# Kernel optimization log

Measured on AMD Instinct MI355X. Metric: run time of the kernel, lower is better.

The kernel has to match this reference:

```python
import jax, jax.numpy as jnp
import numpy as np

B, C, L = 8, 512, 2048
HEADS, DIM_HEAD = 8, 64
HID = HEADS * DIM_HEAD  # 512


def setup_inputs() -> dict:
    key = jax.random.key(0)
    k1, k2, k3, k4 = jax.random.split(key, 4)
    x = jax.random.normal(k1, (B, C, L), dtype=jnp.float32)
    # Conv1d kernel_size=1 weights stored as [out, in] matrices
    w_qkv = jax.random.normal(k2, (3 * HID, C), dtype=jnp.float32) * (1.0 / np.sqrt(C))
    w_out = jax.random.normal(k3, (C, HID), dtype=jnp.float32) * (1.0 / np.sqrt(HID))
    b_out = jax.random.normal(k4, (C,), dtype=jnp.float32) * 0.01
    return {"x": x, "w_qkv": w_qkv, "w_out": w_out, "b_out": b_out}


def reference(x, w_qkv, w_out, b_out):
    scale = DIM_HEAD ** (-0.5)
    # 1x1 conv == channel-wise linear: [b,c,l] -> [b,3*hid,l]
    qkv = jnp.einsum('oc,bcl->bol', w_qkv, x)
    q, k, v = jnp.split(qkv, 3, axis=1)
    # split heads: b (h d) l -> b h d l
    split = lambda t: t.reshape(x.shape[0], HEADS, DIM_HEAD, t.shape[-1])
    q, k, v = split(q) * scale, split(k), split(v)
    sim = jnp.einsum('bhdi,bhdj->bhij', q, k)  # [b,h,l,l]
    attn = jax.nn.softmax(sim, axis=-1)
    out = jnp.einsum('bhij,bhdj->bhid', attn, v)  # [b,h,l,d]
    # b h l d -> b (h d) l
    out = jnp.transpose(out, (0, 1, 3, 2)).reshape(x.shape[0], HID, x.shape[-1])
    return jnp.einsum('oc,bcl->bol', w_out, out) + b_out[None, :, None]
```

## Files before the change

### kernel.cpp

```cpp
#include <hip/hip_runtime.h>

#define NB 8
#define NC 512
#define NL 2048
#define NH 8
#define ND 64
#define NHID 512

typedef float f32x4 __attribute__((ext_vector_type(4)));
typedef short bf16x8 __attribute__((ext_vector_type(8)));
typedef unsigned uint32x2 __attribute__((ext_vector_type(2)));
typedef unsigned uint32x4 __attribute__((ext_vector_type(4)));

__device__ __forceinline__ unsigned short f2bf(float x) {
    unsigned u = __float_as_uint(x);
    u += 0x7fffu + ((u >> 16) & 1u);
    return (unsigned short)(u >> 16);
}

__device__ __forceinline__ unsigned pack_bf16_tr(float lo, float hi) {
#if __has_builtin(__builtin_amdgcn_perm)
    return __builtin_amdgcn_perm(__float_as_uint(hi), __float_as_uint(lo), 0x07060302u);
#else
    return (__float_as_uint(lo) >> 16) | (__float_as_uint(hi) & 0xffff0000u);
#endif
}

__device__ __forceinline__ float fexp2(float x) {
#if __has_builtin(__builtin_amdgcn_exp2f)
    return __builtin_amdgcn_exp2f(x);
#else
    return exp2f(x);
#endif
}

__device__ __forceinline__ void gll16(const unsigned short* g, unsigned short* l) {
    __builtin_amdgcn_global_load_lds(
        (const __attribute__((address_space(1))) unsigned int*)g,
        (__attribute__((address_space(3))) unsigned int*)l, 16, 0, 0);
}

__device__ __forceinline__ void pfr_quad_swap(unsigned &a, unsigned &b) {
#if __has_builtin(__builtin_amdgcn_permlane32_swap) && __has_builtin(__builtin_amdgcn_permlane16_swap)
    uint32x2 r0 = __builtin_amdgcn_permlane32_swap(a, b, false, false);
    uint32x2 r1 = __builtin_amdgcn_permlane16_swap(r0[0], r0[1], false, false);
    a = r1[0];
    b = r1[1];
#else
    const int lane = (int)(threadIdx.x & 63);
    const int li = lane & 15, quad = lane >> 4;
    const int s0 = (li + ((quad & 1) << 5)) << 2;
    const int s1 = (li + 16 + ((quad & 1) << 5)) << 2;
    int ra = __builtin_amdgcn_ds_bpermute(s0, (int)a);
    int rb = __builtin_amdgcn_ds_bpermute(s0, (int)b);
    int ta = __builtin_amdgcn_ds_bpermute(s1, (int)a);
    int tb = __builtin_amdgcn_ds_bpermute(s1, (int)b);
    const bool lo = quad < 2;
    a = (unsigned)(lo ? ra : rb);
    b = (unsigned)(lo ? ta : tb);
#endif
}

__global__ __launch_bounds__(256) void xpose_kernel(
    const float* __restrict__ x, unsigned short* __restrict__ xT)
{
    __shared__ unsigned short T[64 * 65];
    const int tid = threadIdx.x;
    const int l0 = blockIdx.x * 64, c0 = blockIdx.y * 64, b = blockIdx.z;

    const int ll = tid & 63, cl0 = tid >> 6;
    #pragma unroll
    for (int i = 0; i < 16; i++) {
        const int cl = cl0 + 4 * i;
        T[cl * 65 + ll] = f2bf(x[((size_t)(b * NC + c0 + cl)) * NL + l0 + ll]);
    }
    __syncthreads();
    const int cg = tid & 7, lr = tid >> 3;
    #pragma unroll
    for (int rep = 0; rep < 2; rep++) {
        const int l = lr + rep * 32;
        unsigned u[4];
        #pragma unroll
        for (int j = 0; j < 4; j++) {
            unsigned short a = T[(cg * 8 + 2 * j) * 65 + l];
            unsigned short c = T[(cg * 8 + 2 * j + 1) * 65 + l];
            u[j] = (unsigned)a | ((unsigned)c << 16);
        }
        uint4 val; val.x = u[0]; val.y = u[1]; val.z = u[2]; val.w = u[3];
        *(uint4*)&xT[((size_t)(b * NL + l0 + l)) * NC + c0 + cg * 8] = val;
    }
}

__global__ __launch_bounds__(256) void wconv_kernel(
    const float* __restrict__ src, unsigned short* __restrict__ dst,
    int n8, int nscale8, float scale)
{
    const int idx = blockIdx.x * 256 + threadIdx.x;
    if (idx >= n8) return;
    const float s = (idx < nscale8) ? scale : 1.0f;
    float4 a = *(const float4*)&src[(size_t)idx * 8];
    float4 c = *(const float4*)&src[(size_t)idx * 8 + 4];
    uint4 val;
    val.x = (unsigned)f2bf(a.x * s) | ((unsigned)f2bf(a.y * s) << 16);
    val.y = (unsigned)f2bf(a.z * s) | ((unsigned)f2bf(a.w * s) << 16);
    val.z = (unsigned)f2bf(c.x * s) | ((unsigned)f2bf(c.y * s) << 16);
    val.w = (unsigned)f2bf(c.z * s) | ((unsigned)f2bf(c.w * s) << 16);
    *(uint4*)&dst[(size_t)idx * 8] = val;
}

__global__ __launch_bounds__(256) void qkv_proj_kernel(
    const unsigned short* __restrict__ xT, const unsigned short* __restrict__ wq,
    unsigned short* __restrict__ qb, unsigned short* __restrict__ kb,
    unsigned short* __restrict__ vb)
{
    __shared__ __align__(16) unsigned short Xt[128 * 64];
    __shared__ __align__(16) unsigned short Wt[128 * 64];
    const int tid = threadIdx.x;
    const int wave = tid >> 6, lane = tid & 63;
    const int quad = lane >> 4, li = lane & 15;
    const int o0 = blockIdx.x * 128, l0 = blockIdx.y * 128, b = blockIdx.z;

    const f32x4 fzero = {0.f, 0.f, 0.f, 0.f};
    f32x4 acc[2][8];
    #pragma unroll
    for (int mt = 0; mt < 2; mt++)
        #pragma unroll
        for (int nt = 0; nt < 8; nt++) acc[mt][nt] = fzero;

    const int srow = lane >> 3, schk = lane & 7;

    for (int c0 = 0; c0 < NC; c0 += 64) {
        #pragma unroll
        for (int i = 0; i < 4; i++) {
            const int r = wave * 32 + i * 8 + srow;
            gll16(xT + ((size_t)(b * NL + l0 + r)) * NC + c0 + ((schk ^ (r & 7)) * 8),
                  &Xt[(wave * 32 + i * 8) * 64]);
            gll16(wq + (size_t)(o0 + r) * NC + c0 + ((schk ^ (r & 7)) * 8),
                  &Wt[(wave * 32 + i * 8) * 64]);
        }
        __syncthreads();
        #pragma unroll
        for (int kc = 0; kc < 2; kc++) {
            const int sw = ((kc * 4 + quad) ^ (li & 7)) * 8;
            bf16x8 afr0 = *(const bf16x8*)&Xt[(wave * 32 + li) * 64 + sw];
            bf16x8 afr1 = *(const bf16x8*)&Xt[(wave * 32 + 16 + li) * 64 + sw];
            #pragma unroll
            for (int nt = 0; nt < 8; nt++) {
                bf16x8 bfr = *(const bf16x8*)&Wt[(nt * 16 + li) * 64 + sw];
                acc[0][nt] = __builtin_amdgcn_mfma_f32_16x16x32_bf16(afr0, bfr, acc[0][nt], 0, 0, 0);
                acc[1][nt] = __builtin_amdgcn_mfma_f32_16x16x32_bf16(afr1, bfr, acc[1][nt], 0, 0, 0);
            }
        }
        __syncthreads();
    }

    const int lr0 = l0 + wave * 32;
    if (o0 < 1024) {
        unsigned short* dst = (o0 < 512) ? qb : kb;
        #pragma unroll
        for (int mt = 0; mt < 2; mt++)
            #pragma unroll
            for (int nt = 0; nt < 8; nt++) {
                int oc = (o0 & 511) + nt * 16 + li;
                int hh = oc >> 6, d = oc & 63;
                size_t base =
                    ((size_t)((b * NH + hh) * NL) + lr0 + mt * 16 + quad * 4) * ND + d;
                #pragma unroll
                for (int r = 0; r < 4; r++)
                    dst[base + (size_t)r * ND] = f2bf(acc[mt][nt][r]);
            }
    } else {
        #pragma unroll
        for (int mt = 0; mt < 2; mt++)
            #pragma unroll
            for (int nt = 0; nt < 8; nt++) {
                int oc = (o0 - 1024) + nt * 16 + li;
                int hh = oc >> 6, d = oc & 63;
                size_t base = ((size_t)((b * NH + hh) * ND) + d) * NL +
                              lr0 + mt * 16 + quad * 4;
                uint2 pv;
                pv.x = (unsigned)f2bf(acc[mt][nt][0]) | ((unsigned)f2bf(acc[mt][nt][1]) << 16);
                pv.y = (unsigned)f2bf(acc[mt][nt][2]) | ((unsigned)f2bf(acc[mt][nt][3]) << 16);
                *(uint2*)&vb[base] = pv;
            }
    }
}

__global__ __launch_bounds__(256, 4) void attn_kernel(
    const unsigned short* __restrict__ qb, const unsigned short* __restrict__ kb,
    const unsigned short* __restrict__ vb, unsigned short* __restrict__ at)
{
    __shared__ __align__(16) unsigned short Kt[2][64 * 64];
    __shared__ __align__(16) unsigned short Vt[2][64 * 64];
    const int tid = threadIdx.x;
    const int wave = tid >> 6, lane = tid & 63;
    const int quad = lane >> 4, li = lane & 15;

    const int dlin = (int)(blockIdx.x + 16 * (blockIdx.y + 8 * blockIdx.z));
    const int xcd = dlin & 7, slot = dlin >> 3;
    const int qt = slot & 15, gidx = slot >> 4;
    const int g = xcd + 8 * gidx;
    const int h = g & 7, b = g >> 3;

    const int bh = b * NH + h;
    const unsigned short* Qb = qb + (size_t)bh * NL * ND;
    const unsigned short* Kb = kb + (size_t)bh * NL * ND;
    const unsigned short* Vb = vb + (size_t)bh * ND * NL;

    bf16x8 qfr[2][2];
    #pragma unroll
    for (int mt = 0; mt < 2; mt++)
        #pragma unroll
        for (int kc = 0; kc < 2; kc++)
            qfr[mt][kc] = *(const bf16x8*)&Qb[(size_t)(qt * 128 + wave * 32 + mt * 16 + li) * ND +
                                             kc * 32 + quad * 8];

    const f32x4 fzero = {0.f, 0.f, 0.f, 0.f};
    f32x4 oacc[2][4];
    #pragma unroll
    for (int mt = 0; mt < 2; mt++)
        #pragma unroll
        for (int dt = 0; dt < 4; dt++) oacc[mt][dt] = fzero;

    f32x4 lsacc0 = fzero, lsacc1 = fzero;
    const short one_bf = (short)0x3F80;
    const bf16x8 ones = {one_bf, one_bf, one_bf, one_bf,
                         one_bf, one_bf, one_bf, one_bf};

    const int rrow = lane >> 3;
    const int rchk = lane & 7;

    auto stage = [&](int buf, int j0) {
        #pragma unroll
        for (int i = 0; i < 2; i++) {
            const int jrow = wave * 16 + i * 8 + rrow;
            gll16(Kb + (size_t)(j0 + jrow) * ND + ((rchk ^ (jrow & 7)) * 8),
                  &Kt[buf][(wave * 16 + i * 8) * 64]);
            const int drow = wave * 16 + i * 8 + rrow;
            gll16(Vb + (size_t)drow * NL + j0 + ((rchk ^ (drow & 7)) * 8),
                  &Vt[buf][(wave * 16 + i * 8) * 64]);
        }
    };

    stage(0, 0);
    __syncthreads();

    #pragma unroll 2
    for (int kt = 0; kt < 32; kt++) {
        const int cur = kt & 1;
        if (kt < 31) stage(cur ^ 1, (kt + 1) * 64);

        __builtin_amdgcn_s_setprio(1);
        #pragma unroll
        for (int c = 0; c < 2; c++) {
            f32x4 st00 = fzero, st01 = fzero, st10 = fzero, st11 = fzero;
            #pragma unroll
            for (int dk = 0; dk < 2; dk++) {
                const int sw = ((dk * 4 + quad) ^ (li & 7)) * 8;
                bf16x8 kf0 = *(const bf16x8*)&Kt[cur][((2 * c + 0) * 16 + li) * 64 + sw];
                bf16x8 kf1 = *(const bf16x8*)&Kt[cur][((2 * c + 1) * 16 + li) * 64 + sw];
                st00 = __builtin_amdgcn_mfma_f32_16x16x32_bf16(kf0, qfr[0][dk], st00, 0, 0, 0);
                st01 = __builtin_amdgcn_mfma_f32_16x16x32_bf16(kf1, qfr[0][dk], st01, 0, 0, 0);
                st10 = __builtin_amdgcn_mfma_f32_16x16x32_bf16(kf0, qfr[1][dk], st10, 0, 0, 0);
                st11 = __builtin_amdgcn_mfma_f32_16x16x32_bf16(kf1, qfr[1][dk], st11, 0, 0, 0);
            }

            unsigned p000, p001, p010, p011, p100, p101, p110, p111;
            {
                float a0 = fexp2(st00[0]), a1 = fexp2(st00[1]),
                      a2 = fexp2(st00[2]), a3 = fexp2(st00[3]);
                float b0 = fexp2(st01[0]), b1 = fexp2(st01[1]),
                      b2 = fexp2(st01[2]), b3 = fexp2(st01[3]);
                p000 = pack_bf16_tr(a0, a1); p001 = pack_bf16_tr(a2, a3);
                p010 = pack_bf16_tr(b0, b1); p011 = pack_bf16_tr(b2, b3);
            }
            {
                float a0 = fexp2(st10[0]), a1 = fexp2(st10[1]),
                      a2 = fexp2(st10[2]), a3 = fexp2(st10[3]);
                float b0 = fexp2(st11[0]), b1 = fexp2(st11[1]),
                      b2 = fexp2(st11[2]), b3 = fexp2(st11[3]);
                p100 = pack_bf16_tr(a0, a1); p101 = pack_bf16_tr(a2, a3);
                p110 = pack_bf16_tr(b0, b1); p111 = pack_bf16_tr(b2, b3);
            }

            pfr_quad_swap(p000, p010);
            pfr_quad_swap(p001, p011);
            pfr_quad_swap(p100, p110);
            pfr_quad_swap(p101, p111);

            uint32x4 u0 = {p000, p001, p010, p011};
            uint32x4 u1 = {p100, p101, p110, p111};
            bf16x8 pf0 = __builtin_bit_cast(bf16x8, u0);
            bf16x8 pf1 = __builtin_bit_cast(bf16x8, u1);

            lsacc0 = __builtin_amdgcn_mfma_f32_16x16x32_bf16(ones, pf0, lsacc0, 0, 0, 0);
            lsacc1 = __builtin_amdgcn_mfma_f32_16x16x32_bf16(ones, pf1, lsacc1, 0, 0, 0);

            #pragma unroll
            for (int dt = 0; dt < 4; dt++) {
                const int swv = ((c * 4 + quad) ^ (li & 7)) * 8;
                bf16x8 vfr = *(const bf16x8*)&Vt[cur][(dt * 16 + li) * 64 + swv];
                oacc[0][dt] = __builtin_amdgcn_mfma_f32_16x16x32_bf16(vfr, pf0, oacc[0][dt], 0, 0, 0);
                oacc[1][dt] = __builtin_amdgcn_mfma_f32_16x16x32_bf16(vfr, pf1, oacc[1][dt], 0, 0, 0);
            }
        }
        __builtin_amdgcn_s_setprio(0);
        __syncthreads();
    }

    #pragma unroll
    for (int mt = 0; mt < 2; mt++) {
        const float rl = 1.0f / (mt ? lsacc1[0] : lsacc0[0]);
        const int l = qt * 128 + wave * 32 + mt * 16 + li;
        #pragma unroll
        for (int dt = 0; dt < 4; dt++) {
            uint2 ov;
            ov.x = (unsigned)f2bf(oacc[mt][dt][0] * rl) |
                   ((unsigned)f2bf(oacc[mt][dt][1] * rl) << 16);
            ov.y = (unsigned)f2bf(oacc[mt][dt][2] * rl) |
                   ((unsigned)f2bf(oacc[mt][dt][3] * rl) << 16);
            *(uint2*)&at[((size_t)(b * NL + l)) * NHID + h * ND + dt * 16 + quad * 4] = ov;
        }
    }
}

__global__ __launch_bounds__(256) void out_proj_kernel(
    const unsigned short* __restrict__ at, const unsigned short* __restrict__ wo,
    const float* __restrict__ bias, float* __restrict__ out)
{
    __shared__ __align__(16) unsigned short Wt[128 * 64];
    __shared__ __align__(16) unsigned short At[128 * 64];
    const int tid = threadIdx.x;
    const int wave = tid >> 6, lane = tid & 63;
    const int quad = lane >> 4, li = lane & 15;
    const int o0 = blockIdx.x * 128, l0 = blockIdx.y * 128, b = blockIdx.z;

    const f32x4 fzero = {0.f, 0.f, 0.f, 0.f};
    f32x4 acc[2][8];
    #pragma unroll
    for (int mt = 0; mt < 2; mt++)
        #pragma unroll
        for (int nt = 0; nt < 8; nt++) acc[mt][nt] = fzero;

    const int srow = lane >> 3, schk = lane & 7;

    for (int c0 = 0; c0 < NHID; c0 += 64) {
        #pragma unroll
        for (int i = 0; i < 4; i++) {
            const int r = wave * 32 + i * 8 + srow;
            gll16(wo + (size_t)(o0 + r) * NHID + c0 + ((schk ^ (r & 7)) * 8),
                  &Wt[(wave * 32 + i * 8) * 64]);
            gll16(at + ((size_t)(b * NL + l0 + r)) * NHID + c0 + ((schk ^ (r & 7)) * 8),
                  &At[(wave * 32 + i * 8) * 64]);
        }
        __syncthreads();
        #pragma unroll
        for (int kc = 0; kc < 2; kc++) {
            const int sw = ((kc * 4 + quad) ^ (li & 7)) * 8;
            bf16x8 afr0 = *(const bf16x8*)&Wt[(wave * 32 + li) * 64 + sw];
            bf16x8 afr1 = *(const bf16x8*)&Wt[(wave * 32 + 16 + li) * 64 + sw];
            #pragma unroll
            for (int nt = 0; nt < 8; nt++) {
                bf16x8 bfr = *(const bf16x8*)&At[(nt * 16 + li) * 64 + sw];
                acc[0][nt] = __builtin_amdgcn_mfma_f32_16x16x32_bf16(afr0, bfr, acc[0][nt], 0, 0, 0);
                acc[1][nt] = __builtin_amdgcn_mfma_f32_16x16x32_bf16(afr1, bfr, acc[1][nt], 0, 0, 0);
            }
        }
        __syncthreads();
    }

    #pragma unroll
    for (int mt = 0; mt < 2; mt++) {
        int or0 = o0 + wave * 32 + mt * 16 + quad * 4;
        #pragma unroll
        for (int nt = 0; nt < 8; nt++) {
            int l = l0 + nt * 16 + li;
            #pragma unroll
            for (int r = 0; r < 4; r++)
                out[((size_t)(b * NC + or0 + r)) * NL + l] = acc[mt][nt][r] + bias[or0 + r];
        }
    }
}

extern "C" void kernel_launch(void* const* d_in, const int* in_sizes, int n_in,
                              void* d_out, int out_size, void* d_ws, size_t ws_size,
                              hipStream_t stream) {
    const float* x = (const float*)d_in[0];
    const float* w_qkv = (const float*)d_in[1];
    const float* w_out = (const float*)d_in[2];
    const float* b_out = (const float*)d_in[3];
    float* out = (float*)d_out;

    unsigned short* ws = (unsigned short*)d_ws;
    const size_t SZ = (size_t)NB * NH * NL * ND;
    unsigned short* qb = ws;
    unsigned short* kb = qb + SZ;
    unsigned short* vb = kb + SZ;
    unsigned short* at = vb + SZ;
    unsigned short* xT = at + SZ;
    unsigned short* wqb = xT + SZ;
    unsigned short* wob = wqb + (size_t)3 * NHID * NC;

    xpose_kernel<<<dim3(NL / 64, NC / 64, NB), dim3(256), 0, stream>>>(x, xT);
    wconv_kernel<<<dim3((3 * NHID * NC / 8 + 255) / 256), dim3(256), 0, stream>>>(
        w_qkv, wqb, 3 * NHID * NC / 8, NHID * NC / 8, 0.125f * 1.44269504088896f);
    wconv_kernel<<<dim3((NC * NHID / 8 + 255) / 256), dim3(256), 0, stream>>>(
        w_out, wob, NC * NHID / 8, 0, 1.0f);

    qkv_proj_kernel<<<dim3(12, 16, 8), dim3(256), 0, stream>>>(xT, wqb, qb, kb, vb);
    attn_kernel<<<dim3(16, 8, 8), dim3(256), 0, stream>>>(qb, kb, vb, at);
    out_proj_kernel<<<dim3(4, 16, 8), dim3(256), 0, stream>>>(at, wob, b_out, out);
}
```

Before: 222.4 us.

## Double-buffer projection GEMMs, remap blocks across XCDs, fuse weight conversion launches

The QKV and output projection GEMMs now double-buffer their LDS tiles, so the async global-to-LDS load of the next K chunk overlaps the MFMAs on the current one. Both raise wave priority around the MFMA section and remap block indices so blocks that share an input tile land on the same XCD for L2 reuse. The two weight-conversion kernels are merged into one launch to save a launch. In exchange LDS use per block doubles, which can lower occupancy.

```diff
diff --git a/kernel.cpp b/kernel.cpp
--- a/kernel.cpp
+++ b/kernel.cpp
@@ -91,21 +91,33 @@
     }
 }
 
-__global__ __launch_bounds__(256) void wconv_kernel(
-    const float* __restrict__ src, unsigned short* __restrict__ dst,
-    int n8, int nscale8, float scale)
+__global__ __launch_bounds__(256) void wconv_fused_kernel(
+    const float* __restrict__ srcA, unsigned short* __restrict__ dstA,
+    int n8A, int nscale8, float scale,
+    const float* __restrict__ srcB, unsigned short* __restrict__ dstB, int n8B)
 {
     const int idx = blockIdx.x * 256 + threadIdx.x;
-    if (idx >= n8) return;
-    const float s = (idx < nscale8) ? scale : 1.0f;
-    float4 a = *(const float4*)&src[(size_t)idx * 8];
-    float4 c = *(const float4*)&src[(size_t)idx * 8 + 4];
+    const float* src;
+    unsigned short* dst;
+    float s;
+    size_t off;
+    if (idx < n8A) {
+        src = srcA; dst = dstA; off = (size_t)idx * 8;
+        s = (idx < nscale8) ? scale : 1.0f;
+    } else {
+        const int j = idx - n8A;
+        if (j >= n8B) return;
+        src = srcB; dst = dstB; off = (size_t)j * 8;
+        s = 1.0f;
+    }
+    float4 a = *(const float4*)&src[off];
+    float4 c = *(const float4*)&src[off + 4];
     uint4 val;
     val.x = (unsigned)f2bf(a.x * s) | ((unsigned)f2bf(a.y * s) << 16);
     val.y = (unsigned)f2bf(a.z * s) | ((unsigned)f2bf(a.w * s) << 16);
     val.z = (unsigned)f2bf(c.x * s) | ((unsigned)f2bf(c.y * s) << 16);
     val.w = (unsigned)f2bf(c.z * s) | ((unsigned)f2bf(c.w * s) << 16);
-    *(uint4*)&dst[(size_t)idx * 8] = val;
+    *(uint4*)&dst[off] = val;
 }
 
 __global__ __launch_bounds__(256) void qkv_proj_kernel(
@@ -113,12 +125,17 @@
     unsigned short* __restrict__ qb, unsigned short* __restrict__ kb,
     unsigned short* __restrict__ vb)
 {
-    __shared__ __align__(16) unsigned short Xt[128 * 64];
-    __shared__ __align__(16) unsigned short Wt[128 * 64];
+    __shared__ __align__(16) unsigned short Xt[2][128 * 64];
+    __shared__ __align__(16) unsigned short Wt[2][128 * 64];
     const int tid = threadIdx.x;
     const int wave = tid >> 6, lane = tid & 63;
     const int quad = lane >> 4, li = lane & 15;
-    const int o0 = blockIdx.x * 128, l0 = blockIdx.y * 128, b = blockIdx.z;
+
+    const int dlin = (int)(blockIdx.x + 12 * (blockIdx.y + 16 * blockIdx.z));
+    const int xcd = dlin & 7, slot = dlin >> 3;
+    const int ot = slot % 12, pl = slot / 12;
+    const int pg = xcd + 8 * pl;
+    const int o0 = ot * 128, l0 = (pg & 15) * 128, b = pg >> 4;
 
     const f32x4 fzero = {0.f, 0.f, 0.f, 0.f};
     f32x4 acc[2][8];
@@ -129,28 +146,39 @@
 
     const int srow = lane >> 3, schk = lane & 7;
 
-    for (int c0 = 0; c0 < NC; c0 += 64) {
+    auto stage = [&](int buf, int c0) {
         #pragma unroll
         for (int i = 0; i < 4; i++) {
             const int r = wave * 32 + i * 8 + srow;
             gll16(xT + ((size_t)(b * NL + l0 + r)) * NC + c0 + ((schk ^ (r & 7)) * 8),
-                  &Xt[(wave * 32 + i * 8) * 64]);
+                  &Xt[buf][(wave * 32 + i * 8) * 64]);
             gll16(wq + (size_t)(o0 + r) * NC + c0 + ((schk ^ (r & 7)) * 8),
-                  &Wt[(wave * 32 + i * 8) * 64]);
-        }
-        __syncthreads();
+                  &Wt[buf][(wave * 32 + i * 8) * 64]);
+        }
+    };
+
+    stage(0, 0);
+    __syncthreads();
+
+    #pragma unroll 2
+    for (int it = 0; it < 8; it++) {
+        const int cur = it & 1;
+        if (it < 7) stage(cur ^ 1, (it + 1) * 64);
+
+        __builtin_amdgcn_s_setprio(1);
         #pragma unroll
         for (int kc = 0; kc < 2; kc++) {
             const int sw = ((kc * 4 + quad) ^ (li & 7)) * 8;
-            bf16x8 afr0 = *(const bf16x8*)&Xt[(wave * 32 + li) * 64 + sw];
-            bf16x8 afr1 = *(const bf16x8*)&Xt[(wave * 32 + 16 + li) * 64 + sw];
+            bf16x8 afr0 = *(const bf16x8*)&Xt[cur][(wave * 32 + li) * 64 + sw];
+            bf16x8 afr1 = *(const bf16x8*)&Xt[cur][(wave * 32 + 16 + li) * 64 + sw];
             #pragma unroll
             for (int nt = 0; nt < 8; nt++) {
-                bf16x8 bfr = *(const bf16x8*)&Wt[(nt * 16 + li) * 64 + sw];
+                bf16x8 bfr = *(const bf16x8*)&Wt[cur][(nt * 16 + li) * 64 + sw];
                 acc[0][nt] = __builtin_amdgcn_mfma_f32_16x16x32_bf16(afr0, bfr, acc[0][nt], 0, 0, 0);
                 acc[1][nt] = __builtin_amdgcn_mfma_f32_16x16x32_bf16(afr1, bfr, acc[1][nt], 0, 0, 0);
             }
         }
+        __builtin_amdgcn_s_setprio(0);
         __syncthreads();
     }
 
@@ -328,12 +356,17 @@
     const unsigned short* __restrict__ at, const unsigned short* __restrict__ wo,
     const float* __restrict__ bias, float* __restrict__ out)
 {
-    __shared__ __align__(16) unsigned short Wt[128 * 64];
-    __shared__ __align__(16) unsigned short At[128 * 64];
+    __shared__ __align__(16) unsigned short Wt[2][128 * 64];
+    __shared__ __align__(16) unsigned short At[2][128 * 64];
     const int tid = threadIdx.x;
     const int wave = tid >> 6, lane = tid & 63;
     const int quad = lane >> 4, li = lane & 15;
-    const int o0 = blockIdx.x * 128, l0 = blockIdx.y * 128, b = blockIdx.z;
+
+    const int dlin = (int)(blockIdx.x + 4 * (blockIdx.y + 16 * blockIdx.z));
+    const int xcd = dlin & 7, slot = dlin >> 3;
+    const int ot = slot & 3, pl = slot >> 2;
+    const int pg = xcd + 8 * pl;
+    const int o0 = ot * 128, l0 = (pg & 15) * 128, b = pg >> 4;
 
     const f32x4 fzero = {0.f, 0.f, 0.f, 0.f};
     f32x4 acc[2][8];
@@ -344,28 +377,39 @@
 
     const int srow = lane >> 3, schk = lane & 7;
 
-    for (int c0 = 0; c0 < NHID; c0 += 64) {
+    auto stage = [&](int buf, int c0) {
         #pragma unroll
         for (int i = 0; i < 4; i++) {
             const int r = wave * 32 + i * 8 + srow;
             gll16(wo + (size_t)(o0 + r) * NHID + c0 + ((schk ^ (r & 7)) * 8),
-                  &Wt[(wave * 32 + i * 8) * 64]);
+                  &Wt[buf][(wave * 32 + i * 8) * 64]);
             gll16(at + ((size_t)(b * NL + l0 + r)) * NHID + c0 + ((schk ^ (r & 7)) * 8),
-                  &At[(wave * 32 + i * 8) * 64]);
-        }
-        __syncthreads();
+                  &At[buf][(wave * 32 + i * 8) * 64]);
+        }
+    };
+
+    stage(0, 0);
+    __syncthreads();
+
+    #pragma unroll 2
+    for (int it = 0; it < 8; it++) {
+        const int cur = it & 1;
+        if (it < 7) stage(cur ^ 1, (it + 1) * 64);
+
+        __builtin_amdgcn_s_setprio(1);
         #pragma unroll
         for (int kc = 0; kc < 2; kc++) {
             const int sw = ((kc * 4 + quad) ^ (li & 7)) * 8;
-            bf16x8 afr0 = *(const bf16x8*)&Wt[(wave * 32 + li) * 64 + sw];
-            bf16x8 afr1 = *(const bf16x8*)&Wt[(wave * 32 + 16 + li) * 64 + sw];
+            bf16x8 afr0 = *(const bf16x8*)&Wt[cur][(wave * 32 + li) * 64 + sw];
+            bf16x8 afr1 = *(const bf16x8*)&Wt[cur][(wave * 32 + 16 + li) * 64 + sw];
             #pragma unroll
             for (int nt = 0; nt < 8; nt++) {
-                bf16x8 bfr = *(const bf16x8*)&At[(nt * 16 + li) * 64 + sw];
+                bf16x8 bfr = *(const bf16x8*)&At[cur][(nt * 16 + li) * 64 + sw];
                 acc[0][nt] = __builtin_amdgcn_mfma_f32_16x16x32_bf16(afr0, bfr, acc[0][nt], 0, 0, 0);
                 acc[1][nt] = __builtin_amdgcn_mfma_f32_16x16x32_bf16(afr1, bfr, acc[1][nt], 0, 0, 0);
             }
         }
+        __builtin_amdgcn_s_setprio(0);
         __syncthreads();
     }
 
@@ -402,10 +446,13 @@
     unsigned short* wob = wqb + (size_t)3 * NHID * NC;
 
     xpose_kernel<<<dim3(NL / 64, NC / 64, NB), dim3(256), 0, stream>>>(x, xT);
-    wconv_kernel<<<dim3((3 * NHID * NC / 8 + 255) / 256), dim3(256), 0, stream>>>(
-        w_qkv, wqb, 3 * NHID * NC / 8, NHID * NC / 8, 0.125f * 1.44269504088896f);
-    wconv_kernel<<<dim3((NC * NHID / 8 + 255) / 256), dim3(256), 0, stream>>>(
-        w_out, wob, NC * NHID / 8, 0, 1.0f);
+    {
+        const int n8A = 3 * NHID * NC / 8;
+        const int n8B = NC * NHID / 8;
+        wconv_fused_kernel<<<dim3((n8A + n8B + 255) / 256), dim3(256), 0, stream>>>(
+            w_qkv, wqb, n8A, NHID * NC / 8, 0.125f * 1.44269504088896f,
+            w_out, wob, n8B);
+    }
 
     qkv_proj_kernel<<<dim3(12, 16, 8), dim3(256), 0, stream>>>(xT, wqb, qb, kb, vb);
     attn_kernel<<<dim3(16, 8, 8), dim3(256), 0, stream>>>(qb, kb, vb, at);
```

Result: faster. 210.4 us (-5.4%).
